# Performance work log

Hardware: AMD Instinct MI355X
Metric: run time of the kernel (lower is better)

Reference implementation:

```python
import jax, jax.numpy as jnp
import numpy as np

TOP_K = 2


def setup_inputs() -> dict:
    key = jax.random.key(0)
    ks = jax.random.split(key, 5)
    B, S, H, E, F = 4, 1024, 1024, 16, 4096
    scale = 0.02
    return {
        "input_tensor": jax.random.normal(ks[0], (B, S, H), dtype=jnp.float32),
        "Wg": scale * jax.random.normal(ks[1], (H, E), dtype=jnp.float32),
        "bg": jnp.zeros((E,), dtype=jnp.float32),
        "W1": scale * jax.random.normal(ks[2], (E, H, F), dtype=jnp.float32),
        "b1": jnp.zeros((E, F), dtype=jnp.float32),
        "W2": scale * jax.random.normal(ks[3], (E, F, H), dtype=jnp.float32),
        "b2": jnp.zeros((E, H), dtype=jnp.float32),
    }


def reference(input_tensor, Wg, bg, W1, b1, W2, b2):
    # Faithful to DualOutputMoE.forward_first_pass: the per-(b,s,k) Python loop
    # plus _weighted_sum collapses ALL token expert outputs into a single
    # [1,1,H] vector normalized by the total routing weight (= B*S).
    B, S, H = input_tensor.shape
    T = B * S
    E = Wg.shape[1]
    x = input_tensor.reshape(T, H)

    routing_scores = x @ Wg + bg                    # [T, E] (raw gate logits)
    top_v, top_i = jax.lax.top_k(routing_scores, TOP_K)
    top_w = jax.nn.softmax(top_v, axis=-1)          # per-token top-k weights

    # combine[t, e] = sum_k top_w[t, k] * 1[top_i[t, k] == e]
    combine = jnp.zeros((T, E), x.dtype).at[jnp.arange(T)[:, None], top_i].add(top_w)
    total_weight = top_w.sum()                      # matches python sum of .item()s

    def expert_step(acc, params):
        w1, bb1, w2, bb2, c = params                # c: [T] combine weights for this expert
        y = jax.nn.gelu(x @ w1 + bb1, approximate=False) @ w2 + bb2  # [T, H]
        return acc + c @ y, None

    acc0 = jnp.zeros((H,), x.dtype)
    acc, _ = jax.lax.scan(expert_step, acc0, (W1, b1, W2, b2, combine.T))
    first_output = (acc / total_weight).reshape(1, 1, H)
    return first_output
```

## Files before the change

kernel.cpp:

```cpp
#include <hip/hip_runtime.h>
#include <hip/hip_bf16.h>
#include <math.h>

typedef __bf16 bf16_t;
typedef __bf16 bf16x4 __attribute__((ext_vector_type(4)));
typedef __bf16 bf16x8 __attribute__((ext_vector_type(8)));
typedef float  f32x4  __attribute__((ext_vector_type(4)));

#define T_TOK 4096
#define H_DIM 1024
#define E_NUM 16
#define F_DIM 4096
#define CH_ROWS 128
#define CH_MAX  32

#define WS_E0     0
#define WS_E1     16384
#define WS_W0     32768
#define WS_W1     49152
#define WS_COUNTS 65536
#define WS_SUMW   65664
#define WS_XOFF   65792
#define WS_LIDX   131072
#define WS_LW     393216
#define WS_GPART  655360
#define WS_XE     9306112
#define WS_W1T    30277632
#define WS_P2     164495360

#define AS_GLOBAL(p) ((const __attribute__((address_space(1))) void*)(p))
#define AS_LDS(p)    ((__attribute__((address_space(3))) void*)(p))

__global__ __launch_bounds__(256) void k_route(const float* __restrict__ x,
    const float* __restrict__ Wg, const float* __restrict__ bg,
    int* __restrict__ e0, int* __restrict__ e1,
    float* __restrict__ w0, float* __restrict__ w1)
{
    const int t = blockIdx.x * 4 + (threadIdx.x >> 6);
    const int lane = threadIdx.x & 63;
    const float* xr = x + (size_t)t * H_DIM;

    float s[E_NUM];
#pragma unroll
    for (int e = 0; e < E_NUM; ++e) s[e] = 0.f;

#pragma unroll
    for (int i = 0; i < 16; ++i) {
        const int h = i * 64 + lane;
        const float xv = xr[h];
        const float4* wr = (const float4*)(Wg + (size_t)h * E_NUM);
        float4 q0 = wr[0], q1 = wr[1], q2 = wr[2], q3 = wr[3];
        s[0] += xv*q0.x;  s[1] += xv*q0.y;  s[2] += xv*q0.z;  s[3] += xv*q0.w;
        s[4] += xv*q1.x;  s[5] += xv*q1.y;  s[6] += xv*q1.z;  s[7] += xv*q1.w;
        s[8] += xv*q2.x;  s[9] += xv*q2.y;  s[10]+= xv*q2.z;  s[11]+= xv*q2.w;
        s[12]+= xv*q3.x;  s[13]+= xv*q3.y;  s[14]+= xv*q3.z;  s[15]+= xv*q3.w;
    }
#pragma unroll
    for (int off = 32; off >= 1; off >>= 1) {
#pragma unroll
        for (int e = 0; e < E_NUM; ++e) s[e] += __shfl_xor(s[e], off);
    }
    if (lane == 0) {
#pragma unroll
        for (int e = 0; e < E_NUM; ++e) s[e] += bg[e];
        float b1v = -3e38f; int i1 = 0;
#pragma unroll
        for (int e = 0; e < E_NUM; ++e) { if (s[e] > b1v) { b1v = s[e]; i1 = e; } }
        float b2v = -3e38f; int i2 = 0;
#pragma unroll
        for (int e = 0; e < E_NUM; ++e) { if (e != i1 && s[e] > b2v) { b2v = s[e]; i2 = e; } }
        const float ex  = expf(b2v - b1v);
        const float inv = 1.f / (1.f + ex);
        e0[t] = i1; e1[t] = i2;
        w0[t] = inv; w1[t] = ex * inv;
    }
}

__global__ __launch_bounds__(64) void k_lists(const int* __restrict__ e0, const int* __restrict__ e1,
    const float* __restrict__ w0, const float* __restrict__ w1,
    int* __restrict__ lidx, float* __restrict__ lw,
    int* __restrict__ counts, float* __restrict__ sumw)
{
    const int e = blockIdx.x;
    const int lane = threadIdx.x;
    int cnt = 0; float sw = 0.f;
    for (int base = 0; base < T_TOK; base += 64) {
        const int t = base + lane;
        const bool m0 = (e0[t] == e);
        const bool m1 = (e1[t] == e);
        const bool m  = m0 | m1;
        const unsigned long long bal = __ballot(m);
        const int pos = cnt + __popcll(bal & ((1ull << lane) - 1ull));
        if (m) {
            const float w = m0 ? w0[t] : w1[t];
            lidx[e * T_TOK + pos] = t;
            lw[e * T_TOK + pos]   = w;
            sw += w;
        }
        cnt += __popcll(bal);
    }
#pragma unroll
    for (int off = 32; off >= 1; off >>= 1) sw += __shfl_xor(sw, off);
    if (lane == 0) { counts[e] = cnt; sumw[e] = sw; }
}

__global__ void k_scan(const int* __restrict__ counts, int* __restrict__ xoff) {
    if (threadIdx.x == 0) {
        int o = 0;
        for (int e = 0; e < E_NUM; ++e) { xoff[e] = o; o += (counts[e] + CH_ROWS - 1) & ~(CH_ROWS - 1); }
    }
}

__global__ __launch_bounds__(256) void k_gather(const float* __restrict__ x,
    const int* __restrict__ lidx, const int* __restrict__ counts,
    const int* __restrict__ xoff, bf16_t* __restrict__ Xe)
{
    const int chunk = blockIdx.x >> 1;
    const int part  = blockIdx.x & 1;
    const int e = blockIdx.y;
    const int cnt = counts[e];
    const int start = chunk * CH_ROWS;
    if (chunk && start >= cnt) return;
    const int tid = threadIdx.x;
    const size_t base = ((size_t)(xoff[e] >> 7) + chunk) * 131072;

    for (int it = 0; it < 32; ++it) {
        const int u    = part * 8192 + it * 256 + tid;
        const int kt   = u >> 10;
        const int wi   = u & 1023;
        const int rl   = wi >> 3;
        const int c    = wi & 7;
        const int row  = start + rl;
        bf16x8 v8 = {};
        if (row < cnt) {
            const int tok = lidx[e * T_TOK + row];
            const int cp  = c ^ (rl & 7);
            const int k   = kt * 64 + cp * 8;
            const float4 a = *(const float4*)(x + (size_t)tok * H_DIM + k);
            const float4 b = *(const float4*)(x + (size_t)tok * H_DIM + k + 4);
            v8[0]=(bf16_t)a.x; v8[1]=(bf16_t)a.y; v8[2]=(bf16_t)a.z; v8[3]=(bf16_t)a.w;
            v8[4]=(bf16_t)b.x; v8[5]=(bf16_t)b.y; v8[6]=(bf16_t)b.z; v8[7]=(bf16_t)b.w;
        }
        *(bf16x8*)(Xe + base + (size_t)kt * 8192 + rl * 64 + c * 8) = v8;
    }
}

__global__ __launch_bounds__(256, 2) void k_w1t(const float* __restrict__ W1,
    bf16_t* __restrict__ W1T)
{
    const int kt = blockIdx.x;
    const int fb = blockIdx.y;
    const int e  = blockIdx.z;
    const int tid = threadIdx.x;

    __shared__ float S[64 * 256];

    const float* src = W1 + (size_t)e * H_DIM * F_DIM + (size_t)(kt * 64) * F_DIM + fb * 256;

#pragma unroll
    for (int it = 0; it < 16; ++it) {
        const int u  = it * 256 + tid;
        const int k  = u >> 6;
        const int c4 = u & 63;
        const float4 v = *(const float4*)(src + (size_t)k * F_DIM + c4 * 4);
        *(float4*)&S[k * 256 + (c4 ^ (k & 7)) * 4] = v;
    }
    __syncthreads();

    {
        const int f   = tid;
        const int ft  = fb * 2 + (tid >> 7);
        const int fl  = tid & 127;
        const int fsw = fl & 7;
        bf16_t* dst = W1T + ((((size_t)e * 32 + ft) * 16 + kt) * 8192) + fl * 64;
#pragma unroll
        for (int s = 0; s < 8; ++s) {
            const int c = s ^ fsw;
            bf16x8 pk;
#pragma unroll
            for (int q = 0; q < 8; ++q) {
                const int k = c * 8 + q;
                pk[q] = (bf16_t)S[k * 256 + ((f >> 2) ^ (k & 7)) * 4 + (f & 3)];
            }
            *(bf16x8*)&dst[s * 8] = pk;
        }
    }
}

__global__ __launch_bounds__(256, 2) void k_expert(
    const bf16_t* __restrict__ W1T, const float* __restrict__ b1,
    const bf16_t* __restrict__ Xe, const float* __restrict__ lw,
    const int* __restrict__ counts, const int* __restrict__ xoff,
    float* __restrict__ gpart)
{
    const int ftile = blockIdx.x;
    const int chunk = blockIdx.y;
    const int e     = blockIdx.z;
    const int cnt   = counts[e];
    const int start = chunk * CH_ROWS;
    if (chunk && start >= cnt) return;

    __shared__ __align__(16) bf16_t Alds[2][8192];
    __shared__ __align__(16) bf16_t Blds[2][8192];
    __shared__ float w_s[CH_ROWS];
    __shared__ float b1_s[128];
    __shared__ float gred[2][128];

    const int tid  = threadIdx.x;
    const int lane = tid & 63;
    const int wid  = tid >> 6;
    const int wm   = wid & 1;
    const int wn   = wid >> 1;
    const int lr   = lane & 15;
    const int lg   = lane >> 4;

    if (tid < CH_ROWS) {
        const int r = start + tid;
        w_s[tid] = (r < cnt) ? lw[e * T_TOK + r] : 0.f;
    }
    if (tid < 128) b1_s[tid] = b1[(size_t)e * F_DIM + ftile * 128 + tid];

    f32x4 acc[4][4];
#pragma unroll
    for (int i = 0; i < 4; ++i)
#pragma unroll
        for (int j = 0; j < 4; ++j)
#pragma unroll
            for (int q = 0; q < 4; ++q) acc[i][j][q] = 0.f;

    const bf16_t* XeSlab = Xe + ((size_t)(xoff[e] >> 7) + chunk) * 131072;
    const bf16_t* W1Slab = W1T + (((size_t)e * 32 + ftile) * 16) * 8192;

#define STAGE(T, BUF) { \
    const bf16_t* sa = XeSlab + (size_t)(T) * 8192; \
    const bf16_t* sb = W1Slab + (size_t)(T) * 8192; \
    _Pragma("unroll") \
    for (int p = 0; p < 4; ++p) { \
        const int off = p * 2048 + wid * 512; \
        __builtin_amdgcn_global_load_lds(AS_GLOBAL(sa + off + lane * 8), AS_LDS(&Alds[BUF][off]), 16, 0, 0); \
        __builtin_amdgcn_global_load_lds(AS_GLOBAL(sb + off + lane * 8), AS_LDS(&Blds[BUF][off]), 16, 0, 0); \
    } }

#define COMPUTE(BUF) { \
    _Pragma("unroll") \
    for (int kh = 0; kh < 2; ++kh) { \
        bf16x8 af[4], bfr[4]; \
        _Pragma("unroll") \
        for (int mf = 0; mf < 4; ++mf) { \
            const int r = wm * 64 + mf * 16 + lr; \
            af[mf] = *(const bf16x8*)&Alds[BUF][r * 64 + (((kh << 2) | lg) ^ (r & 7)) * 8]; \
        } \
        _Pragma("unroll") \
        for (int nf = 0; nf < 4; ++nf) { \
            const int f = wn * 64 + nf * 16 + lr; \
            bfr[nf] = *(const bf16x8*)&Blds[BUF][f * 64 + (((kh << 2) | lg) ^ (f & 7)) * 8]; \
        } \
        _Pragma("unroll") \
        for (int mf = 0; mf < 4; ++mf) \
            _Pragma("unroll") \
            for (int nf = 0; nf < 4; ++nf) \
                acc[mf][nf] = __builtin_amdgcn_mfma_f32_16x16x32_bf16(af[mf], bfr[nf], acc[mf][nf], 0, 0, 0); \
    } }

    STAGE(0, 0);
    __builtin_amdgcn_sched_barrier(0);

    int cur = 0;
#pragma unroll
    for (int t = 0; t < 16; ++t) {
        if (t < 15) STAGE(t + 1, cur ^ 1);
        __builtin_amdgcn_sched_barrier(0);
        if (t < 15) { asm volatile("s_waitcnt vmcnt(8)" ::: "memory"); }
        else        { asm volatile("s_waitcnt vmcnt(0)" ::: "memory"); }
        __builtin_amdgcn_sched_barrier(0);
        __builtin_amdgcn_s_barrier();
        __builtin_amdgcn_sched_barrier(0);
        COMPUTE(cur);
        __builtin_amdgcn_sched_barrier(0);
        asm volatile("s_waitcnt lgkmcnt(0)" ::: "memory");
        __builtin_amdgcn_s_barrier();
        cur ^= 1;
    }
#undef STAGE
#undef COMPUTE

    float gcol[4] = {0.f, 0.f, 0.f, 0.f};
#pragma unroll
    for (int nf = 0; nf < 4; ++nf) {
        const float bb = b1_s[wn * 64 + nf * 16 + lr];
#pragma unroll
        for (int mf = 0; mf < 4; ++mf) {
#pragma unroll
            for (int i = 0; i < 4; ++i) {
                const int row = wm * 64 + mf * 16 + lg * 4 + i;
                const float h  = acc[mf][nf][i] + bb;
                const float gl = 0.5f * h * (1.f + erff(h * 0.70710678118654752f));
                gcol[nf] += w_s[row] * gl;
            }
        }
    }
#pragma unroll
    for (int nf = 0; nf < 4; ++nf) {
        gcol[nf] += __shfl_xor(gcol[nf], 16);
        gcol[nf] += __shfl_xor(gcol[nf], 32);
    }
    if (lane < 16) {
#pragma unroll
        for (int nf = 0; nf < 4; ++nf) gred[wm][wn * 64 + nf * 16 + lane] = gcol[nf];
    }
    __syncthreads();
    if (tid < 128) {
        const float sum = gred[0][tid] + gred[1][tid];
        gpart[(size_t)(e * CH_MAX + chunk) * F_DIM + ftile * 128 + tid] = sum;
    }
}

__global__ __launch_bounds__(256) void k_out1(const float* __restrict__ gpart,
    const int* __restrict__ counts, const float* __restrict__ W2, float* __restrict__ p2)
{
    const int fc = blockIdx.x;
    const int e  = blockIdx.y;
    const int tid = threadIdx.x;
    __shared__ float gs[128];
    if (tid < 128) {
        const int nch = (counts[e] + CH_ROWS - 1) / CH_ROWS;
        float s = 0.f;
        for (int c = 0; c < nch; ++c)
            s += gpart[(size_t)(e * CH_MAX + c) * F_DIM + fc * 128 + tid];
        gs[tid] = s;
    }
    __syncthreads();
    const float* W2p = W2 + (size_t)e * F_DIM * H_DIM + (size_t)fc * 128 * H_DIM;
    float ax = 0.f, ay = 0.f, az = 0.f, aw = 0.f;
#pragma unroll 8
    for (int f = 0; f < 128; ++f) {
        const float gv = gs[f];
        const float4 wv = *(const float4*)(W2p + (size_t)f * H_DIM + tid * 4);
        ax += gv * wv.x; ay += gv * wv.y; az += gv * wv.z; aw += gv * wv.w;
    }
    float4 st; st.x = ax; st.y = ay; st.z = az; st.w = aw;
    *(float4*)(p2 + (size_t)(e * 32 + fc) * H_DIM + tid * 4) = st;
}

__global__ __launch_bounds__(256) void k_out2(const float* __restrict__ p2,
    const float* __restrict__ sumw, const float* __restrict__ b2, float* __restrict__ out)
{
    const int tid = threadIdx.x;
    const int hh  = tid & 31;
    const int seg = tid >> 5;
    const int h   = blockIdx.x * 32 + hh;
    float s = 0.f;
    for (int j = 0; j < 64; ++j)
        s += p2[(size_t)(seg * 64 + j) * H_DIM + h];
    __shared__ float red[8][33];
    red[seg][hh] = s;
    __syncthreads();
    if (tid < 32) {
        const int h2 = blockIdx.x * 32 + tid;
        float tot = 0.f;
#pragma unroll
        for (int q = 0; q < 8; ++q) tot += red[q][tid];
        float tw = 0.f, bias = 0.f;
#pragma unroll
        for (int e = 0; e < E_NUM; ++e) { tw += sumw[e]; bias += sumw[e] * b2[e * H_DIM + h2]; }
        out[h2] = (tot + bias) / tw;
    }
}

extern "C" void kernel_launch(void* const* d_in, const int* in_sizes, int n_in,
                              void* d_out, int out_size, void* d_ws, size_t ws_size,
                              hipStream_t stream) {
    const float* x  = (const float*)d_in[0];
    const float* Wg = (const float*)d_in[1];
    const float* bg = (const float*)d_in[2];
    const float* W1 = (const float*)d_in[3];
    const float* b1 = (const float*)d_in[4];
    const float* W2 = (const float*)d_in[5];
    const float* b2 = (const float*)d_in[6];
    float* out = (float*)d_out;

    char* ws = (char*)d_ws;
    int*    e0     = (int*)(ws + WS_E0);
    int*    e1     = (int*)(ws + WS_E1);
    float*  w0     = (float*)(ws + WS_W0);
    float*  w1     = (float*)(ws + WS_W1);
    int*    counts = (int*)(ws + WS_COUNTS);
    float*  sumw   = (float*)(ws + WS_SUMW);
    int*    xoff   = (int*)(ws + WS_XOFF);
    int*    lidx   = (int*)(ws + WS_LIDX);
    float*  lw     = (float*)(ws + WS_LW);
    float*  gpart  = (float*)(ws + WS_GPART);
    bf16_t* Xe     = (bf16_t*)(ws + WS_XE);
    bf16_t* W1T    = (bf16_t*)(ws + WS_W1T);
    float*  p2     = (float*)(ws + WS_P2);

    k_route<<<T_TOK / 4, 256, 0, stream>>>(x, Wg, bg, e0, e1, w0, w1);
    k_lists<<<E_NUM, 64, 0, stream>>>(e0, e1, w0, w1, lidx, lw, counts, sumw);
    k_scan<<<1, 64, 0, stream>>>(counts, xoff);
    k_w1t<<<dim3(16, 16, E_NUM), 256, 0, stream>>>(W1, W1T);
    k_gather<<<dim3(CH_MAX * 2, E_NUM), 256, 0, stream>>>(x, lidx, counts, xoff, Xe);
    k_expert<<<dim3(32, CH_MAX, E_NUM), 256, 0, stream>>>(W1T, b1, Xe, lw, counts, xoff, gpart);
    k_out1<<<dim3(32, E_NUM), 256, 0, stream>>>(gpart, counts, W2, p2);
    k_out2<<<32, 256, 0, stream>>>(p2, sumw, b2, out);
}
```

Before: 345.5 us.

## Replace double-buffered LDS pipeline with single buffer and higher occupancy

Removes the explicit double-buffered global-to-LDS prefetch and its hand-placed waitcnt and barriers in the expert GEMM. It now uses one LDS buffer per operand with plain __syncthreads around each load and compute step. Launch bounds go from 2 to 4 blocks per CU. The aim is to hide memory latency by running more resident blocks instead of by software pipelining within one block. In exchange, each block stalls on every tile load, and it relies on the compiler inserting the vmcnt waits the async LDS loads need before the barrier.

```diff
diff --git a/kernel.cpp b/kernel.cpp
--- a/kernel.cpp
+++ b/kernel.cpp
@@ -187,7 +187,7 @@
     }
 }
 
-__global__ __launch_bounds__(256, 2) void k_expert(
+__global__ __launch_bounds__(256, 4) void k_expert(
     const bf16_t* __restrict__ W1T, const float* __restrict__ b1,
     const bf16_t* __restrict__ Xe, const float* __restrict__ lw,
     const int* __restrict__ counts, const int* __restrict__ xoff,
@@ -200,8 +200,8 @@
     const int start = chunk * CH_ROWS;
     if (chunk && start >= cnt) return;
 
-    __shared__ __align__(16) bf16_t Alds[2][8192];
-    __shared__ __align__(16) bf16_t Blds[2][8192];
+    __shared__ __align__(16) bf16_t Alds[8192];
+    __shared__ __align__(16) bf16_t Blds[8192];
     __shared__ float w_s[CH_ROWS];
     __shared__ float b1_s[128];
     __shared__ float gred[2][128];
@@ -231,29 +231,29 @@
     const bf16_t* XeSlab = Xe + ((size_t)(xoff[e] >> 7) + chunk) * 131072;
     const bf16_t* W1Slab = W1T + (((size_t)e * 32 + ftile) * 16) * 8192;
 
-#define STAGE(T, BUF) { \
+#define STAGE(T) { \
     const bf16_t* sa = XeSlab + (size_t)(T) * 8192; \
     const bf16_t* sb = W1Slab + (size_t)(T) * 8192; \
     _Pragma("unroll") \
     for (int p = 0; p < 4; ++p) { \
         const int off = p * 2048 + wid * 512; \
-        __builtin_amdgcn_global_load_lds(AS_GLOBAL(sa + off + lane * 8), AS_LDS(&Alds[BUF][off]), 16, 0, 0); \
-        __builtin_amdgcn_global_load_lds(AS_GLOBAL(sb + off + lane * 8), AS_LDS(&Blds[BUF][off]), 16, 0, 0); \
+        __builtin_amdgcn_global_load_lds(AS_GLOBAL(sa + off + lane * 8), AS_LDS(&Alds[off]), 16, 0, 0); \
+        __builtin_amdgcn_global_load_lds(AS_GLOBAL(sb + off + lane * 8), AS_LDS(&Blds[off]), 16, 0, 0); \
     } }
 
-#define COMPUTE(BUF) { \
+#define COMPUTE() { \
     _Pragma("unroll") \
     for (int kh = 0; kh < 2; ++kh) { \
         bf16x8 af[4], bfr[4]; \
         _Pragma("unroll") \
         for (int mf = 0; mf < 4; ++mf) { \
             const int r = wm * 64 + mf * 16 + lr; \
-            af[mf] = *(const bf16x8*)&Alds[BUF][r * 64 + (((kh << 2) | lg) ^ (r & 7)) * 8]; \
+            af[mf] = *(const bf16x8*)&Alds[r * 64 + (((kh << 2) | lg) ^ (r & 7)) * 8]; \
         } \
         _Pragma("unroll") \
         for (int nf = 0; nf < 4; ++nf) { \
             const int f = wn * 64 + nf * 16 + lr; \
-            bfr[nf] = *(const bf16x8*)&Blds[BUF][f * 64 + (((kh << 2) | lg) ^ (f & 7)) * 8]; \
+            bfr[nf] = *(const bf16x8*)&Blds[f * 64 + (((kh << 2) | lg) ^ (f & 7)) * 8]; \
         } \
         _Pragma("unroll") \
         for (int mf = 0; mf < 4; ++mf) \
@@ -262,24 +262,12 @@
                 acc[mf][nf] = __builtin_amdgcn_mfma_f32_16x16x32_bf16(af[mf], bfr[nf], acc[mf][nf], 0, 0, 0); \
     } }
 
-    STAGE(0, 0);
-    __builtin_amdgcn_sched_barrier(0);
-
-    int cur = 0;
 #pragma unroll
     for (int t = 0; t < 16; ++t) {
-        if (t < 15) STAGE(t + 1, cur ^ 1);
-        __builtin_amdgcn_sched_barrier(0);
-        if (t < 15) { asm volatile("s_waitcnt vmcnt(8)" ::: "memory"); }
-        else        { asm volatile("s_waitcnt vmcnt(0)" ::: "memory"); }
-        __builtin_amdgcn_sched_barrier(0);
-        __builtin_amdgcn_s_barrier();
-        __builtin_amdgcn_sched_barrier(0);
-        COMPUTE(cur);
-        __builtin_amdgcn_sched_barrier(0);
-        asm volatile("s_waitcnt lgkmcnt(0)" ::: "memory");
-        __builtin_amdgcn_s_barrier();
-        cur ^= 1;
+        STAGE(t);
+        __syncthreads();
+        COMPUTE();
+        __syncthreads();
     }
 #undef STAGE
 #undef COMPUTE
```

Result: slower. 411.0 us (+19.0%).

## Loop expert token chunks inside each block instead of a chunk grid dimension

Applied to the files above, without the earlier changes.

The expert GEMM kernel no longer launches one block per (ftile, chunk, expert) with early exit for empty chunks. Each (ftile, expert) block now loops over all 128-row token chunks of its expert and accumulates the weighted GELU column sums in registers. This removes the many empty blocks, the partial-sum buffer and the chunk reduction in k_out1. The cost is less parallelism (512 blocks) and load imbalance, since blocks for heavily routed experts run many more serial passes and W1 tiles are still reloaded on every pass.

```diff
diff --git a/kernel.cpp b/kernel.cpp
--- a/kernel.cpp
+++ b/kernel.cpp
@@ -23,7 +23,7 @@
 #define WS_XOFF   65792
 #define WS_LIDX   131072
 #define WS_LW     393216
-#define WS_GPART  655360
+#define WS_G      655360
 #define WS_XE     9306112
 #define WS_W1T    30277632
 #define WS_P2     164495360
@@ -191,14 +191,12 @@
     const bf16_t* __restrict__ W1T, const float* __restrict__ b1,
     const bf16_t* __restrict__ Xe, const float* __restrict__ lw,
     const int* __restrict__ counts, const int* __restrict__ xoff,
-    float* __restrict__ gpart)
+    float* __restrict__ g)
 {
     const int ftile = blockIdx.x;
-    const int chunk = blockIdx.y;
-    const int e     = blockIdx.z;
+    const int e     = blockIdx.y;
     const int cnt   = counts[e];
-    const int start = chunk * CH_ROWS;
-    if (chunk && start >= cnt) return;
+    const int npass = (cnt + CH_ROWS - 1) >> 7;
 
     __shared__ __align__(16) bf16_t Alds[2][8192];
     __shared__ __align__(16) bf16_t Blds[2][8192];
@@ -214,25 +212,15 @@
     const int lr   = lane & 15;
     const int lg   = lane >> 4;
 
-    if (tid < CH_ROWS) {
-        const int r = start + tid;
-        w_s[tid] = (r < cnt) ? lw[e * T_TOK + r] : 0.f;
-    }
     if (tid < 128) b1_s[tid] = b1[(size_t)e * F_DIM + ftile * 128 + tid];
 
-    f32x4 acc[4][4];
-#pragma unroll
-    for (int i = 0; i < 4; ++i)
-#pragma unroll
-        for (int j = 0; j < 4; ++j)
-#pragma unroll
-            for (int q = 0; q < 4; ++q) acc[i][j][q] = 0.f;
-
-    const bf16_t* XeSlab = Xe + ((size_t)(xoff[e] >> 7) + chunk) * 131072;
     const bf16_t* W1Slab = W1T + (((size_t)e * 32 + ftile) * 16) * 8192;
-
-#define STAGE(T, BUF) { \
-    const bf16_t* sa = XeSlab + (size_t)(T) * 8192; \
+    const size_t  xeblk  = (size_t)(xoff[e] >> 7);
+
+    float gcol[4] = {0.f, 0.f, 0.f, 0.f};
+
+#define STAGE(T, BUF, XS) { \
+    const bf16_t* sa = (XS) + (size_t)(T) * 8192; \
     const bf16_t* sb = W1Slab + (size_t)(T) * 8192; \
     _Pragma("unroll") \
     for (int p = 0; p < 4; ++p) { \
@@ -262,73 +250,85 @@
                 acc[mf][nf] = __builtin_amdgcn_mfma_f32_16x16x32_bf16(af[mf], bfr[nf], acc[mf][nf], 0, 0, 0); \
     } }
 
-    STAGE(0, 0);
-    __builtin_amdgcn_sched_barrier(0);
-
-    int cur = 0;
-#pragma unroll
-    for (int t = 0; t < 16; ++t) {
-        if (t < 15) STAGE(t + 1, cur ^ 1);
-        __builtin_amdgcn_sched_barrier(0);
-        if (t < 15) { asm volatile("s_waitcnt vmcnt(8)" ::: "memory"); }
-        else        { asm volatile("s_waitcnt vmcnt(0)" ::: "memory"); }
-        __builtin_amdgcn_sched_barrier(0);
-        __builtin_amdgcn_s_barrier();
-        __builtin_amdgcn_sched_barrier(0);
-        COMPUTE(cur);
-        __builtin_amdgcn_sched_barrier(0);
-        asm volatile("s_waitcnt lgkmcnt(0)" ::: "memory");
-        __builtin_amdgcn_s_barrier();
-        cur ^= 1;
+    for (int c = 0; c < npass; ++c) {
+        const int start = c * CH_ROWS;
+        __syncthreads();
+        if (tid < CH_ROWS) {
+            const int r = start + tid;
+            w_s[tid] = (r < cnt) ? lw[e * T_TOK + r] : 0.f;
+        }
+        const bf16_t* XeSlab = Xe + (xeblk + c) * 131072;
+
+        f32x4 acc[4][4];
+#pragma unroll
+        for (int i = 0; i < 4; ++i)
+#pragma unroll
+            for (int j = 0; j < 4; ++j)
+#pragma unroll
+                for (int q = 0; q < 4; ++q) acc[i][j][q] = 0.f;
+
+        STAGE(0, 0, XeSlab);
+        __syncthreads();
+
+        int cur = 0;
+#pragma unroll
+        for (int t = 0; t < 16; ++t) {
+            if (t < 15) STAGE(t + 1, cur ^ 1, XeSlab);
+            __builtin_amdgcn_sched_barrier(0);
+            if (t < 15) { asm volatile("s_waitcnt vmcnt(8)" ::: "memory"); }
+            else        { asm volatile("s_waitcnt vmcnt(0)" ::: "memory"); }
+            __builtin_amdgcn_sched_barrier(0);
+            __builtin_amdgcn_s_barrier();
+            __builtin_amdgcn_sched_barrier(0);
+            COMPUTE(cur);
+            __builtin_amdgcn_sched_barrier(0);
+            asm volatile("s_waitcnt lgkmcnt(0)" ::: "memory");
+            __builtin_amdgcn_s_barrier();
+            cur ^= 1;
+        }
+
+#pragma unroll
+        for (int nf = 0; nf < 4; ++nf) {
+            const float bb = b1_s[wn * 64 + nf * 16 + lr];
+#pragma unroll
+            for (int mf = 0; mf < 4; ++mf) {
+#pragma unroll
+                for (int i = 0; i < 4; ++i) {
+                    const int row = wm * 64 + mf * 16 + lg * 4 + i;
+                    const float h  = acc[mf][nf][i] + bb;
+                    const float gl = 0.5f * h * (1.f + erff(h * 0.70710678118654752f));
+                    gcol[nf] += w_s[row] * gl;
+                }
+            }
+        }
     }
 #undef STAGE
 #undef COMPUTE
 
-    float gcol[4] = {0.f, 0.f, 0.f, 0.f};
-#pragma unroll
-    for (int nf = 0; nf < 4; ++nf) {
-        const float bb = b1_s[wn * 64 + nf * 16 + lr];
-#pragma unroll
-        for (int mf = 0; mf < 4; ++mf) {
-#pragma unroll
-            for (int i = 0; i < 4; ++i) {
-                const int row = wm * 64 + mf * 16 + lg * 4 + i;
-                const float h  = acc[mf][nf][i] + bb;
-                const float gl = 0.5f * h * (1.f + erff(h * 0.70710678118654752f));
-                gcol[nf] += w_s[row] * gl;
-            }
-        }
-    }
 #pragma unroll
     for (int nf = 0; nf < 4; ++nf) {
         gcol[nf] += __shfl_xor(gcol[nf], 16);
         gcol[nf] += __shfl_xor(gcol[nf], 32);
     }
+    __syncthreads();
     if (lane < 16) {
 #pragma unroll
         for (int nf = 0; nf < 4; ++nf) gred[wm][wn * 64 + nf * 16 + lane] = gcol[nf];
     }
     __syncthreads();
     if (tid < 128) {
-        const float sum = gred[0][tid] + gred[1][tid];
-        gpart[(size_t)(e * CH_MAX + chunk) * F_DIM + ftile * 128 + tid] = sum;
-    }
-}
-
-__global__ __launch_bounds__(256) void k_out1(const float* __restrict__ gpart,
-    const int* __restrict__ counts, const float* __restrict__ W2, float* __restrict__ p2)
+        g[(size_t)e * F_DIM + ftile * 128 + tid] = gred[0][tid] + gred[1][tid];
+    }
+}
+
+__global__ __launch_bounds__(256) void k_out1(const float* __restrict__ g,
+    const float* __restrict__ W2, float* __restrict__ p2)
 {
     const int fc = blockIdx.x;
     const int e  = blockIdx.y;
     const int tid = threadIdx.x;
     __shared__ float gs[128];
-    if (tid < 128) {
-        const int nch = (counts[e] + CH_ROWS - 1) / CH_ROWS;
-        float s = 0.f;
-        for (int c = 0; c < nch; ++c)
-            s += gpart[(size_t)(e * CH_MAX + c) * F_DIM + fc * 128 + tid];
-        gs[tid] = s;
-    }
+    if (tid < 128) gs[tid] = g[(size_t)e * F_DIM + fc * 128 + tid];
     __syncthreads();
     const float* W2p = W2 + (size_t)e * F_DIM * H_DIM + (size_t)fc * 128 * H_DIM;
     float ax = 0.f, ay = 0.f, az = 0.f, aw = 0.f;
@@ -389,7 +389,7 @@
     int*    xoff   = (int*)(ws + WS_XOFF);
     int*    lidx   = (int*)(ws + WS_LIDX);
     float*  lw     = (float*)(ws + WS_LW);
-    float*  gpart  = (float*)(ws + WS_GPART);
+    float*  g      = (float*)(ws + WS_G);
     bf16_t* Xe     = (bf16_t*)(ws + WS_XE);
     bf16_t* W1T    = (bf16_t*)(ws + WS_W1T);
     float*  p2     = (float*)(ws + WS_P2);
@@ -399,7 +399,7 @@
     k_scan<<<1, 64, 0, stream>>>(counts, xoff);
     k_w1t<<<dim3(16, 16, E_NUM), 256, 0, stream>>>(W1, W1T);
     k_gather<<<dim3(CH_MAX * 2, E_NUM), 256, 0, stream>>>(x, lidx, counts, xoff, Xe);
-    k_expert<<<dim3(32, CH_MAX, E_NUM), 256, 0, stream>>>(W1T, b1, Xe, lw, counts, xoff, gpart);
-    k_out1<<<dim3(32, E_NUM), 256, 0, stream>>>(gpart, counts, W2, p2);
+    k_expert<<<dim3(32, E_NUM), 256, 0, stream>>>(W1T, b1, Xe, lw, counts, xoff, g);
+    k_out1<<<dim3(32, E_NUM), 256, 0, stream>>>(g, W2, p2);
     k_out2<<<32, 256, 0, stream>>>(p2, sumw, b2, out);
 }
```

After: 477.4 us. 38.2% more time.
